# Optimization experiments

Measured on AMD Instinct MI355X. Metric: run time of the kernel, lower is better.

Reference implementation:

```python
import jax, jax.numpy as jnp
import numpy as np

N, DEG, F_IN, F_OUT = 100000, 16, 128, 128
E = N * DEG


def setup_inputs() -> dict:
    key = jax.random.key(0)
    k0, k1, k2, k3 = jax.random.split(key, 4)
    x = jax.random.normal(k0, (N, F_IN), dtype=jnp.float32)
    # ragged neighbor list flattened: each node has DEG neighbors (sorted segment ids)
    neighbor_feats = jax.random.normal(k1, (E, F_IN), dtype=jnp.float32)
    segment_ids = jnp.repeat(jnp.arange(N, dtype=jnp.int32), DEG)
    # nn.Linear(in, out, bias=False) weights, stored [out, in] as in torch
    Wx = jax.random.normal(k2, (F_OUT, F_IN), dtype=jnp.float32) / np.float32(np.sqrt(F_IN))
    Wn = jax.random.normal(k3, (F_OUT, F_IN), dtype=jnp.float32) / np.float32(np.sqrt(F_IN))
    return {"x": x, "neighbor_feats": neighbor_feats, "segment_ids": segment_ids,
            "Wx": Wx, "Wn": Wn}


def reference(x, neighbor_feats, segment_ids, Wx, Wn):
    n_nodes = x.shape[0]
    # MeanAggregator: per-node mean over its neighbor rows (segment mean)
    sums = jax.ops.segment_sum(neighbor_feats, segment_ids, num_segments=n_nodes)
    counts = jax.ops.segment_sum(
        jnp.ones((neighbor_feats.shape[0],), dtype=x.dtype), segment_ids,
        num_segments=n_nodes)
    f = sums / jnp.maximum(counts, 1.0)[:, None]  # [N, F_IN]
    # tranx(x) + trann(f)
    x_out = x @ Wx.T + f @ Wn.T                   # [N, F_OUT]
    # neighbor = [tranx(n) for n in neighbor], flattened
    nb_out = neighbor_feats @ Wx.T                # [E, F_OUT]
    return x_out, nb_out
```

## Files before the change

### kernel.cpp

```cpp
#include <hip/hip_runtime.h>
#include <stdint.h>
#include <stddef.h>

#define N_NODES 100000
#define F_DIM   128
#define DEG     16
#define N_EDGES (N_NODES*DEG)
#define ROWS_PER_TILE 128
#define N_TILES (N_EDGES/ROWS_PER_TILE)
#define NODES_PER_TILE (ROWS_PER_TILE/DEG)
#define GRID_BLOCKS 2048
#define BLOCK_THREADS 256

typedef __bf16 bf16;
typedef __bf16 bf16x8 __attribute__((ext_vector_type(8)));
typedef float  f32x4  __attribute__((ext_vector_type(4)));

#define WX_BASE 0
#define WN_BASE (128*128)
#define F_BASE  (2*128*128)
#define LDS_ELEMS (2*128*128 + 16*128)

__device__ __forceinline__ int swz(int row, int col) {
  return row*128 + (col ^ ((row & 7) << 3));
}

__device__ __forceinline__ bf16x8 cvt8(f32x4 a, f32x4 b) {
  bf16x8 v;
  v[0]=(bf16)a[0]; v[1]=(bf16)a[1]; v[2]=(bf16)a[2]; v[3]=(bf16)a[3];
  v[4]=(bf16)b[0]; v[5]=(bf16)b[1]; v[6]=(bf16)b[2]; v[7]=(bf16)b[3];
  return v;
}

__device__ __forceinline__ bf16x8 load_frag_g(const float* __restrict__ p) {
  f32x4 a = *(const f32x4*)p;
  f32x4 b = *(const f32x4*)(p + 4);
  return cvt8(a, b);
}

__global__ __launch_bounds__(BLOCK_THREADS, 2)
void feattrans_kernel(const float* __restrict__ x,
                      const float* __restrict__ nb,
                      const float* __restrict__ Wx,
                      const float* __restrict__ Wn,
                      float* __restrict__ out)
{
  __shared__ bf16 lds[LDS_ELEMS];
  const int tid  = threadIdx.x;
  const int wave = tid >> 6;
  const int lane = tid & 63;
  const int l15  = lane & 15;
  const int lk   = lane >> 4;

  #pragma unroll
  for (int it = 0; it < 16; ++it) {
    int idx = it * BLOCK_THREADS + tid;
    int mat = idx >> 11;
    int rem = idx & 2047;
    int row = rem >> 4;
    int g   = rem & 15;
    const float* src = (mat ? Wn : Wx) + row*128 + g*8;
    bf16x8 v = load_frag_g(src);
    *(bf16x8*)&lds[(mat ? WN_BASE : WX_BASE) + swz(row, g*8)] = v;
  }
  __syncthreads();

  float* out_x  = out;
  float* out_nb = out + (size_t)N_NODES * F_DIM;

  for (int tile = blockIdx.x; tile < N_TILES; tile += GRID_BLOCKS) {
    const size_t erow0 = (size_t)tile * ROWS_PER_TILE;

    #pragma unroll
    for (int q = 0; q < 4; ++q) {
      int flat = q * BLOCK_THREADS + tid;
      int node = flat >> 7;
      int col  = flat & 127;
      const float* p = nb + (erow0 + (size_t)node*DEG) * F_DIM + col;
      float s = 0.f;
      #pragma unroll
      for (int r = 0; r < DEG; ++r) s += p[(size_t)r * F_DIM];
      s *= (1.0f / DEG);
      lds[F_BASE + swz(node, col)] = (bf16)s;
    }
    __syncthreads();

    bf16x8 afr[2][4];
    #pragma unroll
    for (int mt = 0; mt < 2; ++mt)
      #pragma unroll
      for (int ks = 0; ks < 4; ++ks) {
        const float* p = nb + (erow0 + wave*32 + mt*16 + l15) * F_DIM + ks*32 + lk*8;
        afr[mt][ks] = load_frag_g(p);
      }

    f32x4 acc[2][8] = {};
    #pragma unroll
    for (int nt = 0; nt < 8; ++nt) {
      int n = nt*16 + l15;
      #pragma unroll
      for (int ks = 0; ks < 4; ++ks) {
        bf16x8 bfr = *(bf16x8*)&lds[WX_BASE + swz(n, ks*32 + lk*8)];
        acc[0][nt] = __builtin_amdgcn_mfma_f32_16x16x32_bf16(afr[0][ks], bfr, acc[0][nt], 0, 0, 0);
        acc[1][nt] = __builtin_amdgcn_mfma_f32_16x16x32_bf16(afr[1][ks], bfr, acc[1][nt], 0, 0, 0);
      }
    }

    #pragma unroll
    for (int mt = 0; mt < 2; ++mt)
      #pragma unroll
      for (int nt = 0; nt < 8; ++nt)
        #pragma unroll
        for (int i = 0; i < 4; ++i) {
          size_t r = erow0 + wave*32 + mt*16 + lk*4 + i;
          out_nb[r * F_DIM + nt*16 + l15] = acc[mt][nt][i];
        }

    const int nodebase = tile * NODES_PER_TILE;
    int xrow = nodebase + l15;
    if (xrow > N_NODES - 1) xrow = N_NODES - 1;

    bf16x8 xfr[4], ffr[4];
    #pragma unroll
    for (int ks = 0; ks < 4; ++ks) {
      xfr[ks] = load_frag_g(x + (size_t)xrow * F_DIM + ks*32 + lk*8);
      ffr[ks] = *(bf16x8*)&lds[F_BASE + swz(l15, ks*32 + lk*8)];
    }

    f32x4 xacc[2] = {};
    #pragma unroll
    for (int j = 0; j < 2; ++j) {
      int nt = wave*2 + j;
      int n  = nt*16 + l15;
      #pragma unroll
      for (int ks = 0; ks < 4; ++ks) {
        bf16x8 bx = *(bf16x8*)&lds[WX_BASE + swz(n, ks*32 + lk*8)];
        bf16x8 bn = *(bf16x8*)&lds[WN_BASE + swz(n, ks*32 + lk*8)];
        xacc[j] = __builtin_amdgcn_mfma_f32_16x16x32_bf16(xfr[ks], bx, xacc[j], 0, 0, 0);
        xacc[j] = __builtin_amdgcn_mfma_f32_16x16x32_bf16(ffr[ks], bn, xacc[j], 0, 0, 0);
      }
    }
    #pragma unroll
    for (int j = 0; j < 2; ++j)
      #pragma unroll
      for (int i = 0; i < 4; ++i) {
        int r = lk*4 + i;
        if (r < NODES_PER_TILE)
          out_x[(size_t)(nodebase + r) * F_DIM + (wave*2 + j)*16 + l15] = xacc[j][i];
      }

    __syncthreads();
  }
}

extern "C" void kernel_launch(void* const* d_in, const int* in_sizes, int n_in,
                              void* d_out, int out_size, void* d_ws, size_t ws_size,
                              hipStream_t stream) {
  const float* x  = (const float*)d_in[0];
  const float* nb = (const float*)d_in[1];
  const float* Wx = (const float*)d_in[3];
  const float* Wn = (const float*)d_in[4];
  float* out = (float*)d_out;

  feattrans_kernel<<<dim3(GRID_BLOCKS), dim3(BLOCK_THREADS), 0, stream>>>(x, nb, Wx, Wn, out);
}
```

Before: 383.8 us.

## Compute neighbor mean via Wn MFMA on loaded fragments instead of re-reading edges

Drops the separate pass that re-read all 16 neighbor rows per node from global memory to build the segment mean. Instead it applies Wn to the already loaded bf16 neighbor fragments with MFMA, then reduces over the 16 rows per node with in-register sums and cross-lane shuffles. The result goes through a small float LDS buffer and is added to the x·Wx output. This removes a second full read of neighbor_feats but doubles the MFMA work on the edge tile. It also changes rounding, since each neighbor row is cast to bf16 before the mean instead of the fp32 mean being cast once.

```diff
diff --git a/kernel.cpp b/kernel.cpp
--- a/kernel.cpp
+++ b/kernel.cpp
@@ -11,15 +11,11 @@
 #define NODES_PER_TILE (ROWS_PER_TILE/DEG)
 #define GRID_BLOCKS 2048
 #define BLOCK_THREADS 256
+#define G_STRIDE 132
 
 typedef __bf16 bf16;
 typedef __bf16 bf16x8 __attribute__((ext_vector_type(8)));
 typedef float  f32x4  __attribute__((ext_vector_type(4)));
-
-#define WX_BASE 0
-#define WN_BASE (128*128)
-#define F_BASE  (2*128*128)
-#define LDS_ELEMS (2*128*128 + 16*128)
 
 __device__ __forceinline__ int swz(int row, int col) {
   return row*128 + (col ^ ((row & 7) << 3));
@@ -45,7 +41,9 @@
                       const float* __restrict__ Wn,
                       float* __restrict__ out)
 {
-  __shared__ bf16 lds[LDS_ELEMS];
+  __shared__ bf16  w_lds[2*128*128];
+  __shared__ float g_lds[16*G_STRIDE];
+
   const int tid  = threadIdx.x;
   const int wave = tid >> 6;
   const int lane = tid & 63;
@@ -61,7 +59,7 @@
     int g   = rem & 15;
     const float* src = (mat ? Wn : Wx) + row*128 + g*8;
     bf16x8 v = load_frag_g(src);
-    *(bf16x8*)&lds[(mat ? WN_BASE : WX_BASE) + swz(row, g*8)] = v;
+    *(bf16x8*)&w_lds[mat*16384 + swz(row, g*8)] = v;
   }
   __syncthreads();
 
@@ -70,20 +68,6 @@
 
   for (int tile = blockIdx.x; tile < N_TILES; tile += GRID_BLOCKS) {
     const size_t erow0 = (size_t)tile * ROWS_PER_TILE;
-
-    #pragma unroll
-    for (int q = 0; q < 4; ++q) {
-      int flat = q * BLOCK_THREADS + tid;
-      int node = flat >> 7;
-      int col  = flat & 127;
-      const float* p = nb + (erow0 + (size_t)node*DEG) * F_DIM + col;
-      float s = 0.f;
-      #pragma unroll
-      for (int r = 0; r < DEG; ++r) s += p[(size_t)r * F_DIM];
-      s *= (1.0f / DEG);
-      lds[F_BASE + swz(node, col)] = (bf16)s;
-    }
-    __syncthreads();
 
     bf16x8 afr[2][4];
     #pragma unroll
@@ -97,15 +81,13 @@
     f32x4 acc[2][8] = {};
     #pragma unroll
     for (int nt = 0; nt < 8; ++nt) {
-      int n = nt*16 + l15;
       #pragma unroll
       for (int ks = 0; ks < 4; ++ks) {
-        bf16x8 bfr = *(bf16x8*)&lds[WX_BASE + swz(n, ks*32 + lk*8)];
+        bf16x8 bfr = *(bf16x8*)&w_lds[swz(nt*16 + l15, ks*32 + lk*8)];
         acc[0][nt] = __builtin_amdgcn_mfma_f32_16x16x32_bf16(afr[0][ks], bfr, acc[0][nt], 0, 0, 0);
         acc[1][nt] = __builtin_amdgcn_mfma_f32_16x16x32_bf16(afr[1][ks], bfr, acc[1][nt], 0, 0, 0);
       }
     }
-
     #pragma unroll
     for (int mt = 0; mt < 2; ++mt)
       #pragma unroll
@@ -116,28 +98,46 @@
           out_nb[r * F_DIM + nt*16 + l15] = acc[mt][nt][i];
         }
 
+    #pragma unroll
+    for (int mt = 0; mt < 2; ++mt) {
+      f32x4 a2[8] = {};
+      #pragma unroll
+      for (int nt = 0; nt < 8; ++nt)
+        #pragma unroll
+        for (int ks = 0; ks < 4; ++ks) {
+          bf16x8 bfr = *(bf16x8*)&w_lds[16384 + swz(nt*16 + l15, ks*32 + lk*8)];
+          a2[nt] = __builtin_amdgcn_mfma_f32_16x16x32_bf16(afr[mt][ks], bfr, a2[nt], 0, 0, 0);
+        }
+      const int gnode = 2*wave + mt;
+      #pragma unroll
+      for (int nt = 0; nt < 8; ++nt) {
+        float s = a2[nt][0] + a2[nt][1] + a2[nt][2] + a2[nt][3];
+        s += __shfl_xor(s, 16, 64);
+        s += __shfl_xor(s, 32, 64);
+        s *= (1.0f / DEG);
+        if ((nt >> 1) == lk)
+          g_lds[gnode*G_STRIDE + nt*16 + l15] = s;
+      }
+    }
+
     const int nodebase = tile * NODES_PER_TILE;
     int xrow = nodebase + l15;
     if (xrow > N_NODES - 1) xrow = N_NODES - 1;
+    bf16x8 xfr[4];
+    #pragma unroll
+    for (int ks = 0; ks < 4; ++ks)
+      xfr[ks] = load_frag_g(x + (size_t)xrow * F_DIM + ks*32 + lk*8);
 
-    bf16x8 xfr[4], ffr[4];
-    #pragma unroll
-    for (int ks = 0; ks < 4; ++ks) {
-      xfr[ks] = load_frag_g(x + (size_t)xrow * F_DIM + ks*32 + lk*8);
-      ffr[ks] = *(bf16x8*)&lds[F_BASE + swz(l15, ks*32 + lk*8)];
-    }
+    __syncthreads();
 
     f32x4 xacc[2] = {};
     #pragma unroll
     for (int j = 0; j < 2; ++j) {
-      int nt = wave*2 + j;
-      int n  = nt*16 + l15;
+      int n = (wave*2 + j)*16 + l15;
       #pragma unroll
       for (int ks = 0; ks < 4; ++ks) {
-        bf16x8 bx = *(bf16x8*)&lds[WX_BASE + swz(n, ks*32 + lk*8)];
-        bf16x8 bn = *(bf16x8*)&lds[WN_BASE + swz(n, ks*32 + lk*8)];
+        bf16x8 bx = *(bf16x8*)&w_lds[swz(n, ks*32 + lk*8)];
         xacc[j] = __builtin_amdgcn_mfma_f32_16x16x32_bf16(xfr[ks], bx, xacc[j], 0, 0, 0);
-        xacc[j] = __builtin_amdgcn_mfma_f32_16x16x32_bf16(ffr[ks], bn, xacc[j], 0, 0, 0);
       }
     }
     #pragma unroll
@@ -145,8 +145,10 @@
       #pragma unroll
       for (int i = 0; i < 4; ++i) {
         int r = lk*4 + i;
-        if (r < NODES_PER_TILE)
-          out_x[(size_t)(nodebase + r) * F_DIM + (wave*2 + j)*16 + l15] = xacc[j][i];
+        if (r < NODES_PER_TILE) {
+          float g = g_lds[r*G_STRIDE + (wave*2 + j)*16 + l15];
+          out_x[(size_t)(nodebase + r) * F_DIM + (wave*2 + j)*16 + l15] = xacc[j][i] + g;
+        }
       }
 
     __syncthreads();
```

Result: faster. 363.6 us, median of 2 (-5.3%).
